# Kernel tuning notes

Measured on AMD Instinct MI355X. Metric: run time of the kernel, lower is better.

## Reference

```python
import jax, jax.numpy as jnp
import numpy as np

R = 2  # p-norm order, matches init kwarg r=2
NUM_CLASSES = 13  # hardcoded in the original forward


def setup_inputs() -> dict:
    key = jax.random.key(0)
    k1, k2, k3, k4, k5 = jax.random.split(key, 5)
    N = 262144
    inp = jax.random.uniform(k1, (N, NUM_CLASSES), dtype=jnp.float32)
    target = jax.random.randint(k2, (N,), 0, NUM_CLASSES, dtype=jnp.int64)
    s = jax.random.normal(k3, (N, NUM_CLASSES), dtype=jnp.float32)
    C_matrix = jax.random.normal(k4, (N, NUM_CLASSES, NUM_CLASSES), dtype=jnp.float32)
    instance_weights = jax.random.uniform(k5, (N,), dtype=jnp.float32)
    return {"input": inp, "target": target, "s": s, "C_matrix": C_matrix,
            "instance_weights": instance_weights}


def _pnorm(x, r, axis):
    # torch.norm(x, r, dim) for float r: (sum |x|^r)^(1/r)
    return jnp.sum(jnp.abs(x) ** r, axis=axis) ** (1.0 / r)


def reference(input, target, s, C_matrix, instance_weights):
    # one-hot scatter of targets: p[n, target[n]] = 1
    p = jax.nn.one_hot(target, NUM_CLASSES, dtype=input.dtype)  # [N,13]
    # batched matvec: C_matrix [N,13,13] @ p [N,13] -> [N,13]
    z_pe = jnp.einsum('nij,nj->ni', C_matrix, p)
    z_p = s - z_pe
    z_p_norm = _pnorm(z_p, R, axis=1)  # [N]
    z_ye = jnp.einsum('nij,nj->ni', C_matrix, input)
    z_y = s - z_ye
    z_y_norm = _pnorm(z_y, R, axis=1)  # [N]
    # diag(z_y @ z_p^T) == row-wise dot product (original wastefully builds NxN)
    diag = jnp.sum(z_y * z_p, axis=1)  # [N]
    return jnp.sum(z_p_norm - diag / z_y_norm)
```

## Files before the change

### kernel.cpp

```cpp
#include <hip/hip_runtime.h>
#include <hip/hip_bf16.h>

#define NCLS 13
#define ROWS_PER_TILE 64
#define BLOCK 256
#define TILES_PER_BLOCK 2


__global__ __launch_bounds__(BLOCK) void rnorm_kernel(
    const float* __restrict__ input,
    const int* __restrict__ target,
    const float* __restrict__ s,
    const float* __restrict__ C,
    float* __restrict__ out,
    int N)
{
    __shared__ float4 c_lds4[2704];
    __shared__ float4 x_lds4[208];
    __shared__ float4 s_lds4[208];
    __shared__ float  wsum[4];

    const float* c_lds = (const float*)c_lds4;
    const float* x_lds = (const float*)x_lds4;
    const float* s_lds = (const float*)s_lds4;

    const int tid = threadIdx.x;
    const int row_local = tid >> 2;
    const int q = tid & 3;

    const int ntiles = N / ROWS_PER_TILE;
    float res_acc = 0.0f;

    for (int tt = 0; tt < TILES_PER_BLOCK; ++tt) {
        const int tile = blockIdx.x * TILES_PER_BLOCK + tt;
        if (tile >= ntiles) break;
        const int base_row = tile * ROWS_PER_TILE;

        const float4* csrc = (const float4*)(C + (size_t)base_row * (NCLS * NCLS));
        for (int k = tid; k < 2704; k += BLOCK)
            c_lds4[k] = csrc[k];
        if (tid < 208) {
            const float4* xsrc = (const float4*)(input + (size_t)base_row * NCLS);
            const float4* ssrc = (const float4*)(s + (size_t)base_row * NCLS);
            x_lds4[tid] = xsrc[tid];
            s_lds4[tid] = ssrc[tid];
        }
        __syncthreads();

        const int t = target[base_row + row_local];

        float xr[NCLS];
#pragma unroll
        for (int j = 0; j < NCLS; ++j) xr[j] = x_lds[row_local * NCLS + j];

        const float* crow = c_lds + row_local * (NCLS * NCLS);
        float sp = 0.0f, sy = 0.0f, dd = 0.0f;

#pragma unroll
        for (int ii = 0; ii < 3; ++ii) {
            const int i = q + 4 * ii;
            float zye = 0.0f, zpe = 0.0f;
#pragma unroll
            for (int j = 0; j < NCLS; ++j) {
                const float c = crow[i * NCLS + j];
                zye = fmaf(c, xr[j], zye);
                if (j == t) zpe = c;
            }
            const float svi = s_lds[row_local * NCLS + i];
            const float zp = svi - zpe;
            const float zy = svi - zye;
            sp = fmaf(zp, zp, sp);
            sy = fmaf(zy, zy, sy);
            dd = fmaf(zy, zp, dd);
        }
        if (q == 0) {
            const int i = 12;
            float zye = 0.0f, zpe = 0.0f;
#pragma unroll
            for (int j = 0; j < NCLS; ++j) {
                const float c = crow[i * NCLS + j];
                zye = fmaf(c, xr[j], zye);
                if (j == t) zpe = c;
            }
            const float svi = s_lds[row_local * NCLS + i];
            const float zp = svi - zpe;
            const float zy = svi - zye;
            sp = fmaf(zp, zp, sp);
            sy = fmaf(zy, zy, sy);
            dd = fmaf(zy, zp, dd);
        }

        sp += __shfl_xor(sp, 1); sp += __shfl_xor(sp, 2);
        sy += __shfl_xor(sy, 1); sy += __shfl_xor(sy, 2);
        dd += __shfl_xor(dd, 1); dd += __shfl_xor(dd, 2);

        if (q == 0)
            res_acc += sqrtf(sp) - dd / sqrtf(sy);

        __syncthreads();
    }

#pragma unroll
    for (int off = 32; off > 0; off >>= 1)
        res_acc += __shfl_down(res_acc, off, 64);

    const int lane = tid & 63;
    const int wid  = tid >> 6;
    if (lane == 0) wsum[wid] = res_acc;
    __syncthreads();
    if (tid == 0) {
        atomicAdd(out, wsum[0] + wsum[1] + wsum[2] + wsum[3]);
    }
}

extern "C" void kernel_launch(void* const* d_in, const int* in_sizes, int n_in,
                              void* d_out, int out_size, void* d_ws, size_t ws_size,
                              hipStream_t stream) {
    const float* input  = (const float*)d_in[0];
    const int*   target = (const int*)d_in[1];
    const float* s      = (const float*)d_in[2];
    const float* C      = (const float*)d_in[3];

    float* out = (float*)d_out;
    int N = in_sizes[1];

    hipMemsetAsync(out, 0, sizeof(float) * out_size, stream);

    const int ntiles = N / ROWS_PER_TILE;
    const int grid = (ntiles + TILES_PER_BLOCK - 1) / TILES_PER_BLOCK;
    rnorm_kernel<<<grid, BLOCK, 0, stream>>>(input, target, s, C, out, N);
}
```

Measured before the change: 59.76 us.

## Double-buffer tiles with async global-to-LDS loads and 8 threads per row

Replaces the synchronous register-staged copy of C, input and s into shared memory with direct global-to-LDS async loads (global_load_lds) into a double buffer. The next tile is prefetched while the current one is computed. Tiles shrink to 32 rows, each row is split across 8 threads instead of 4, and each block processes 8 tiles. The goal is to hide HBM latency in a bandwidth-bound kernel, at the cost of a full vmcnt(0) wait per tile and fewer resident blocks because of the larger LDS footprint.

After: 48.33 us. 1.24x faster.

```diff
diff --git a/kernel.cpp b/kernel.cpp
--- a/kernel.cpp
+++ b/kernel.cpp
@@ -2,10 +2,35 @@
 #include <hip/hip_bf16.h>
 
 #define NCLS 13
-#define ROWS_PER_TILE 64
+#define ROWS 32
 #define BLOCK 256
-#define TILES_PER_BLOCK 2
+#define TPB 8
+#define C_FLOATS (ROWS * NCLS * NCLS)
+#define XS_FLOATS (ROWS * NCLS)
+#define C_F4 (C_FLOATS / 4)
+#define XS_F4 (XS_FLOATS / 4)
 
+__device__ __forceinline__ void async_cp16(const float* g, float* l) {
+    __builtin_amdgcn_global_load_lds(
+        (__attribute__((address_space(1))) void*)(const_cast<float*>(g)),
+        (__attribute__((address_space(3))) void*)(l),
+        16, 0, 0);
+}
+
+__device__ __forceinline__ void stage_tile(float* cb, float* xb, float* sb,
+                                           const float* Cg, const float* xg,
+                                           const float* sg, int tid) {
+#pragma unroll
+    for (int m = 0; m < 6; ++m) {
+        int k = m * BLOCK + tid;
+        if (k < C_F4)
+            async_cp16(Cg + (size_t)k * 4, cb + (size_t)k * 4);
+    }
+    if (tid < XS_F4)
+        async_cp16(xg + (size_t)tid * 4, xb + (size_t)tid * 4);
+    else if (tid >= 128 && tid < 128 + XS_F4)
+        async_cp16(sg + (size_t)(tid - 128) * 4, sb + (size_t)(tid - 128) * 4);
+}
 
 __global__ __launch_bounds__(BLOCK) void rnorm_kernel(
     const float* __restrict__ input,
@@ -13,91 +38,94 @@
     const float* __restrict__ s,
     const float* __restrict__ C,
     float* __restrict__ out,
-    int N)
+    int ntiles)
 {
-    __shared__ float4 c_lds4[2704];
-    __shared__ float4 x_lds4[208];
-    __shared__ float4 s_lds4[208];
-    __shared__ float  wsum[4];
-
-    const float* c_lds = (const float*)c_lds4;
-    const float* x_lds = (const float*)x_lds4;
-    const float* s_lds = (const float*)s_lds4;
+    __shared__ __align__(16) float cbuf[2][C_FLOATS];
+    __shared__ __align__(16) float xbuf[2][XS_FLOATS];
+    __shared__ __align__(16) float sbuf[2][XS_FLOATS];
+    __shared__ float wsum[4];
 
     const int tid = threadIdx.x;
-    const int row_local = tid >> 2;
-    const int q = tid & 3;
+    const int row = tid >> 3;
+    const int q   = tid & 7;
 
-    const int ntiles = N / ROWS_PER_TILE;
+    const int tile0 = blockIdx.x * TPB;
+    const int nt = min(TPB, ntiles - tile0);
     float res_acc = 0.0f;
 
-    for (int tt = 0; tt < TILES_PER_BLOCK; ++tt) {
-        const int tile = blockIdx.x * TILES_PER_BLOCK + tt;
-        if (tile >= ntiles) break;
-        const int base_row = tile * ROWS_PER_TILE;
-
-        const float4* csrc = (const float4*)(C + (size_t)base_row * (NCLS * NCLS));
-        for (int k = tid; k < 2704; k += BLOCK)
-            c_lds4[k] = csrc[k];
-        if (tid < 208) {
-            const float4* xsrc = (const float4*)(input + (size_t)base_row * NCLS);
-            const float4* ssrc = (const float4*)(s + (size_t)base_row * NCLS);
-            x_lds4[tid] = xsrc[tid];
-            s_lds4[tid] = ssrc[tid];
-        }
+    if (nt > 0) {
+        stage_tile(cbuf[0], xbuf[0], sbuf[0],
+                   C + (size_t)tile0 * C_FLOATS,
+                   input + (size_t)tile0 * XS_FLOATS,
+                   s + (size_t)tile0 * XS_FLOATS, tid);
+        int t_cur = target[tile0 * ROWS + row];
+        asm volatile("s_waitcnt vmcnt(0)" ::: "memory");
         __syncthreads();
 
-        const int t = target[base_row + row_local];
+        for (int t = 0; t < nt; ++t) {
+            const int cur = t & 1;
+            const float* cb = cbuf[cur];
+            const float* xb = xbuf[cur];
+            const float* sb = sbuf[cur];
 
-        float xr[NCLS];
+            int t_next = 0;
+            if (t + 1 < nt) {
+                const int tile = tile0 + t + 1;
+                stage_tile(cbuf[cur ^ 1], xbuf[cur ^ 1], sbuf[cur ^ 1],
+                           C + (size_t)tile * C_FLOATS,
+                           input + (size_t)tile * XS_FLOATS,
+                           s + (size_t)tile * XS_FLOATS, tid);
+                t_next = target[tile * ROWS + row];
+            }
+
+            float xr[NCLS];
 #pragma unroll
-        for (int j = 0; j < NCLS; ++j) xr[j] = x_lds[row_local * NCLS + j];
+            for (int j = 0; j < NCLS; ++j) xr[j] = xb[row * NCLS + j];
 
-        const float* crow = c_lds + row_local * (NCLS * NCLS);
-        float sp = 0.0f, sy = 0.0f, dd = 0.0f;
+            const float* crow = cb + row * (NCLS * NCLS);
+            float sp = 0.0f, sy = 0.0f, dd = 0.0f;
+            const int tt = t_cur;
 
+            {
+                const int i = q;
+                float zye = 0.0f, zpe = 0.0f;
 #pragma unroll
-        for (int ii = 0; ii < 3; ++ii) {
-            const int i = q + 4 * ii;
-            float zye = 0.0f, zpe = 0.0f;
+                for (int j = 0; j < NCLS; ++j) {
+                    const float c = crow[i * NCLS + j];
+                    zye = fmaf(c, xr[j], zye);
+                    if (j == tt) zpe = c;
+                }
+                const float svi = sb[row * NCLS + i];
+                const float zp = svi - zpe, zy = svi - zye;
+                sp = fmaf(zp, zp, sp); sy = fmaf(zy, zy, sy); dd = fmaf(zy, zp, dd);
+            }
+            if (q < 5) {
+                const int i = q + 8;
+                float zye = 0.0f, zpe = 0.0f;
 #pragma unroll
-            for (int j = 0; j < NCLS; ++j) {
-                const float c = crow[i * NCLS + j];
-                zye = fmaf(c, xr[j], zye);
-                if (j == t) zpe = c;
+                for (int j = 0; j < NCLS; ++j) {
+                    const float c = crow[i * NCLS + j];
+                    zye = fmaf(c, xr[j], zye);
+                    if (j == tt) zpe = c;
+                }
+                const float svi = sb[row * NCLS + i];
+                const float zp = svi - zpe, zy = svi - zye;
+                sp = fmaf(zp, zp, sp); sy = fmaf(zy, zy, sy); dd = fmaf(zy, zp, dd);
             }
-            const float svi = s_lds[row_local * NCLS + i];
-            const float zp = svi - zpe;
-            const float zy = svi - zye;
-            sp = fmaf(zp, zp, sp);
-            sy = fmaf(zy, zy, sy);
-            dd = fmaf(zy, zp, dd);
+
+            sp += __shfl_xor(sp, 1); sp += __shfl_xor(sp, 2); sp += __shfl_xor(sp, 4);
+            sy += __shfl_xor(sy, 1); sy += __shfl_xor(sy, 2); sy += __shfl_xor(sy, 4);
+            dd += __shfl_xor(dd, 1); dd += __shfl_xor(dd, 2); dd += __shfl_xor(dd, 4);
+
+            if (q == 0)
+                res_acc += sqrtf(sp) - dd / sqrtf(sy);
+
+            if (t + 1 < nt) {
+                asm volatile("s_waitcnt vmcnt(0)" ::: "memory");
+                __syncthreads();
+                t_cur = t_next;
+            }
         }
-        if (q == 0) {
-            const int i = 12;
-            float zye = 0.0f, zpe = 0.0f;
-#pragma unroll
-            for (int j = 0; j < NCLS; ++j) {
-                const float c = crow[i * NCLS + j];
-                zye = fmaf(c, xr[j], zye);
-                if (j == t) zpe = c;
-            }
-            const float svi = s_lds[row_local * NCLS + i];
-            const float zp = svi - zpe;
-            const float zy = svi - zye;
-            sp = fmaf(zp, zp, sp);
-            sy = fmaf(zy, zy, sy);
-            dd = fmaf(zy, zp, dd);
-        }
-
-        sp += __shfl_xor(sp, 1); sp += __shfl_xor(sp, 2);
-        sy += __shfl_xor(sy, 1); sy += __shfl_xor(sy, 2);
-        dd += __shfl_xor(dd, 1); dd += __shfl_xor(dd, 2);
-
-        if (q == 0)
-            res_acc += sqrtf(sp) - dd / sqrtf(sy);
-
-        __syncthreads();
     }
 
 #pragma unroll
@@ -108,9 +136,8 @@
     const int wid  = tid >> 6;
     if (lane == 0) wsum[wid] = res_acc;
     __syncthreads();
-    if (tid == 0) {
+    if (tid == 0)
         atomicAdd(out, wsum[0] + wsum[1] + wsum[2] + wsum[3]);
-    }
 }
 
 extern "C" void kernel_launch(void* const* d_in, const int* in_sizes, int n_in,
@@ -126,7 +153,7 @@
 
     hipMemsetAsync(out, 0, sizeof(float) * out_size, stream);
 
-    const int ntiles = N / ROWS_PER_TILE;
-    const int grid = (ntiles + TILES_PER_BLOCK - 1) / TILES_PER_BLOCK;
-    rnorm_kernel<<<grid, BLOCK, 0, stream>>>(input, target, s, C, out, N);
+    const int ntiles = N / ROWS;
+    const int grid = (ntiles + TPB - 1) / TPB;
+    rnorm_kernel<<<grid, BLOCK, 0, stream>>>(input, target, s, C, out, ntiles);
 }
```
